# Optimization experiments

Hardware: AMD Instinct MI355X
Metric: run time of the kernel (lower is better)

The kernel has to match this reference:

```python
import jax, jax.numpy as jnp
import numpy as np

N = 100000      # nodes
E = 1600000     # edges
F_IN = 128      # num_features
H = 64          # hidden_channels
EPS = 1e-5      # batchnorm eps


def _bn(x, gamma, beta, mean, var):
    # inference-mode BatchNorm1d
    return (x - mean) * jax.lax.rsqrt(var + EPS) * gamma + beta


def setup_inputs() -> dict:
    key = jax.random.key(0)
    ks = jax.random.split(key, 16)

    def lin_w(k, fan_in, fan_out):
        return (jax.random.normal(k, (fan_in, fan_out), jnp.float32)
                * (1.0 / np.sqrt(fan_in)))

    return {
        "x": jax.random.normal(ks[0], (N, F_IN), jnp.float32),
        "edge_index": jax.random.randint(ks[1], (2, E), 0, N, dtype=jnp.int32),
        # node_encoder: Linear(F_IN,H) + BN
        "enc_W": lin_w(ks[2], F_IN, H), "enc_b": jnp.zeros((H,), jnp.float32),
        "enc_g": jnp.ones((H,), jnp.float32), "enc_beta": jnp.zeros((H,), jnp.float32),
        "enc_mean": jnp.zeros((H,), jnp.float32), "enc_var": jnp.ones((H,), jnp.float32),
        # GCNConv layers (PyG: lin without bias, bias added after aggregation)
        "conv1_W": lin_w(ks[3], H, H), "conv1_b": jnp.zeros((H,), jnp.float32),
        "conv2_W": lin_w(ks[4], H, H), "conv2_b": jnp.zeros((H,), jnp.float32),
        # edge_predictor: Linear(2H,H) + BN + Linear(H,1)
        "ep1_W": lin_w(ks[5], 2 * H, H), "ep1_b": jnp.zeros((H,), jnp.float32),
        "ep_g": jnp.ones((H,), jnp.float32), "ep_beta": jnp.zeros((H,), jnp.float32),
        "ep_mean": jnp.zeros((H,), jnp.float32), "ep_var": jnp.ones((H,), jnp.float32),
        "ep2_W": lin_w(ks[6], H, 1), "ep2_b": jnp.zeros((1,), jnp.float32),
    }


def reference(x, edge_index, enc_W, enc_b, enc_g, enc_beta, enc_mean, enc_var,
              conv1_W, conv1_b, conv2_W, conv2_b,
              ep1_W, ep1_b, ep_g, ep_beta, ep_mean, ep_var, ep2_W, ep2_b):
    row, col = edge_index[0], edge_index[1]

    # GCN normalization with added self-loops (symmetric D^-1/2 (A+I) D^-1/2)
    loops = jnp.arange(N, dtype=row.dtype)
    row_sl = jnp.concatenate([row, loops])          # [E+N]
    col_sl = jnp.concatenate([col, loops])
    deg = jax.ops.segment_sum(jnp.ones_like(col_sl, jnp.float32), col_sl, N)
    dinv = jnp.where(deg > 0, jax.lax.rsqrt(jnp.maximum(deg, 1.0)), 0.0)
    norm = dinv[row_sl] * dinv[col_sl]              # [E+N]

    def gcn_conv(h, W, b):
        hw = h @ W                                   # [N,H]
        msg = hw[row_sl] * norm[:, None]             # gather-scale  [E+N,H]
        return jax.ops.segment_sum(msg, col_sl, N) + b  # scatter-add

    # node encoder (inference: dropout = identity)
    h = jax.nn.relu(_bn(x @ enc_W + enc_b, enc_g, enc_beta, enc_mean, enc_var))
    h = jax.nn.relu(gcn_conv(h, conv1_W, conv1_b))
    h = jax.nn.relu(gcn_conv(h, conv2_W, conv2_b))
    node_embeddings = h

    # edge predictor: gather + cat + MLP + sigmoid
    ef = jnp.concatenate([h[row], h[col]], axis=1)   # [E, 2H]
    e = jax.nn.relu(_bn(ef @ ep1_W + ep1_b, ep_g, ep_beta, ep_mean, ep_var))
    edge_pred = jax.nn.sigmoid(e @ ep2_W + ep2_b)    # [E, 1]
    return node_embeddings, edge_pred
```

## Files before the change

### kernel.cpp

```cpp
#include <hip/hip_runtime.h>
#include <hip/hip_bf16.h>
#include <hip/hip_fp16.h>

#define NN 100000
#define NE 1600000
#define FIN 128
#define HD 64
#define NB_SCAN 391
#define NB_MF 1563
#define BSH 9
#define NBUCK 196
#define BCAP 10240
#define CHUNK 4096
#define NCHUNK 391
#define ESPLIT 4
#define NEB (NBUCK*ESPLIT)
#define NFB 6250

typedef unsigned int uint32;
typedef _Float16 half8 __attribute__((ext_vector_type(8)));
typedef float f32x4 __attribute__((ext_vector_type(4)));
typedef float f32x8 __attribute__((ext_vector_type(8)));

__global__ void __launch_bounds__(256) k_part(const int* __restrict__ row,
                                              const int* __restrict__ col,
                                              int* __restrict__ bcnt,
                                              uint32* __restrict__ staged,
                                              uint32* __restrict__ posE){
    __shared__ int hist[NBUCK];
    __shared__ int base[NBUCK];
    int t = threadIdx.x;
    int e0 = blockIdx.x * CHUNK;
    int e1 = min(e0 + CHUNK, NE);
    for(int i = t; i < NBUCK; i += 256) hist[i] = 0;
    __syncthreads();
    for(int e = e0 + t; e < e1; e += 256)
        atomicAdd(&hist[col[e] >> BSH], 1);
    __syncthreads();
    for(int i = t; i < NBUCK; i += 256){
        int c = hist[i];
        base[i] = (c > 0) ? atomicAdd(&bcnt[i], c) : 0;
        hist[i] = 0;
    }
    __syncthreads();
    for(int e = e0 + t; e < e1; e += 256){
        int c = col[e], r = row[e];
        int b = c >> BSH;
        int pos = base[b] + atomicAdd(&hist[b], 1);
        if(pos < BCAP){
            staged[(size_t)b*BCAP + pos] = ((uint32)r << BSH) | (uint32)(c & 511);
            posE[e] = (uint32)(b*BCAP + pos);
        } else posE[e] = 0xFFFFFFFFu;
    }
}

__global__ void __launch_bounds__(256) k_hist(const int* __restrict__ bcnt,
                                              const uint32* __restrict__ staged,
                                              int* __restrict__ deg){
    __shared__ int h[512];
    int b = blockIdx.x, t = threadIdx.x;
    for(int i = t; i < 512; i += 256) h[i] = 0;
    __syncthreads();
    int cnt = min(bcnt[b], BCAP);
    const uint32* st = staged + (size_t)b*BCAP;
    for(int i = t; i < cnt; i += 256) atomicAdd(&h[st[i] & 511u], 1);
    __syncthreads();
    for(int i = t; i < 512; i += 256){
        int n = b*512 + i;
        if(n < NN) deg[n] = h[i];
    }
}

__global__ void k_bsum(const int* __restrict__ deg, int* __restrict__ bsum){
    __shared__ int r[256];
    int t = threadIdx.x; int i = blockIdx.x*256 + t;
    r[t] = (i < NN) ? deg[i] : 0;
    __syncthreads();
    for(int off=128; off>0; off>>=1){ if(t<off) r[t]+=r[t+off]; __syncthreads(); }
    if(t==0) bsum[blockIdx.x] = r[0];
}

__global__ void k_top(int* __restrict__ bsum){
    __shared__ int s[512];
    int t = threadIdx.x;
    int v = (t < NB_SCAN) ? bsum[t] : 0;
    s[t] = v; __syncthreads();
    for(int off=1; off<512; off<<=1){
        int a = (t>=off)? s[t-off] : 0;
        __syncthreads();
        s[t] += a;
        __syncthreads();
    }
    if(t < NB_SCAN) bsum[t] = s[t] - v;
}

__global__ void k_scan(const int* __restrict__ deg, const int* __restrict__ bsum,
                       int* __restrict__ starts, float* __restrict__ dinv){
    __shared__ int s[256];
    int t = threadIdx.x; int i = blockIdx.x*256 + t;
    int d = (i<NN)? deg[i] : 0;
    s[t] = d; __syncthreads();
    for(int off=1; off<256; off<<=1){
        int a = (t>=off)? s[t-off] : 0;
        __syncthreads();
        s[t] += a;
        __syncthreads();
    }
    if(i < NN){
        starts[i] = bsum[blockIdx.x] + s[t] - d;
        dinv[i] = rsqrtf((float)(d + 1));
    }
}

__global__ void __launch_bounds__(256) k_fill2(const int* __restrict__ bcnt,
                                               const uint32* __restrict__ staged,
                                               const int* __restrict__ starts,
                                               int* __restrict__ csr){
    __shared__ int cur[512];
    __shared__ int lcsr[BCAP];
    int b = blockIdx.x, t = threadIdx.x;
    int n0 = b*512;
    int base = starts[n0];
    for(int i = t; i < 512; i += 256){
        int n = n0 + i;
        cur[i] = (n < NN) ? starts[n] - base : 0;
    }
    __syncthreads();
    int cnt = min(bcnt[b], BCAP);
    const uint32* st = staged + (size_t)b*BCAP;
    for(int i = t; i < cnt; i += 256){
        uint32 u = st[i];
        int p = atomicAdd(&cur[u & 511u], 1);
        lcsr[p] = (int)(u >> BSH);
    }
    __syncthreads();
    for(int i = t; i < cnt; i += 256) csr[base + i] = lcsr[i];
}

__global__ void k_const(const float* __restrict__ encB, const float* __restrict__ encG,
                        const float* __restrict__ encBe, const float* __restrict__ encM,
                        const float* __restrict__ encV,
                        const float* __restrict__ ep1b, const float* __restrict__ epG,
                        const float* __restrict__ epBe, const float* __restrict__ epM,
                        const float* __restrict__ epV,
                        float* __restrict__ foldEnc, float* __restrict__ foldPre){
    int j = threadIdx.x;
    if(j < 64){
        float s = encG[j]*rsqrtf(encV[j]+1e-5f);
        foldEnc[j]      = s;
        foldEnc[64+j]   = (encB[j]-encM[j])*s + encBe[j];
        float sp = epG[j]*rsqrtf(epV[j]+1e-5f);
        foldPre[j]      = sp;
        foldPre[64+j]   = sp;
        foldPre[128+j]  = sp*(ep1b[j]-epM[j]) + epBe[j];
        foldPre[192+j]  = 0.f;
    }
}

__global__ void k_wprep(const float* __restrict__ encW, const float* __restrict__ c1W,
                        const float* __restrict__ c2W, const float* __restrict__ ep1W,
                        _Float16* __restrict__ wt){
    int i = blockIdx.x*256 + threadIdx.x;
    if(i < 8192){
        int n = i >> 7, k = i & 127;
        wt[i] = (_Float16)encW[k*64 + n];
    } else if(i < 12288){
        int j = i - 8192; int n = j >> 6, k = j & 63;
        wt[i] = (_Float16)c1W[k*64 + n];
    } else if(i < 16384){
        int j = i - 12288; int n = j >> 6, k = j & 63;
        wt[i] = (_Float16)c2W[k*64 + n];
    } else if(i < 24576){
        int j = i - 16384; int h = j >> 12; int jj = j & 4095;
        int n = jj >> 6, k = jj & 63;
        wt[i] = (_Float16)ep1W[(h*64 + k)*64 + n];
    }
}

template<int K, bool AF32, bool FOLD, bool RELU, bool SCALE, int OS>
__global__ void __launch_bounds__(256) k_mfma(const void* __restrict__ Ain,
                                              const _Float16* __restrict__ Bt,
                                              const float* __restrict__ fold,
                                              const float* __restrict__ rowscale,
                                              _Float16* __restrict__ outh){
    constexpr int PS = K + 8;
    __shared__ _Float16 As[64*PS];
    __shared__ _Float16 Bs[64*PS];
    int t = threadIdx.x;
    int m0 = blockIdx.x*64;
    int jh = blockIdx.y;
    {
        const _Float16* src = Bt + (size_t)jh*64*K;
        for(int idx = t; idx < 64*(K/8); idx += 256){
            int n = idx/(K/8), c = idx%(K/8);
            *(half8*)&Bs[n*PS + c*8] = *(const half8*)&src[n*K + c*8];
        }
    }
    if(AF32){
        const float* A = (const float*)Ain;
        for(int idx = t; idx < 64*(K/4); idx += 256){
            int r = idx/(K/4), c = idx%(K/4);
            int rowi = m0 + r; if(rowi >= NN) rowi = NN-1;
            float4 v = *(const float4*)&A[(size_t)rowi*K + c*4];
            _Float16* d = &As[r*PS + c*4];
            d[0]=(_Float16)v.x; d[1]=(_Float16)v.y; d[2]=(_Float16)v.z; d[3]=(_Float16)v.w;
        }
    } else {
        const _Float16* A = (const _Float16*)Ain;
        for(int idx = t; idx < 64*(K/8); idx += 256){
            int r = idx/(K/8), c = idx%(K/8);
            int rowi = m0 + r; if(rowi >= NN) rowi = NN-1;
            *(half8*)&As[r*PS + c*8] = *(const half8*)&A[(size_t)rowi*K + c*8];
        }
    }
    __syncthreads();
    int w = t>>6, l = t&63;
    int lm = l&15, q = l>>4;
    f32x4 acc0 = {0.f,0.f,0.f,0.f}, acc1 = {0.f,0.f,0.f,0.f};
    f32x4 acc2 = {0.f,0.f,0.f,0.f}, acc3 = {0.f,0.f,0.f,0.f};
    const _Float16* arow = &As[(w*16+lm)*PS + q*8];
    const _Float16* brow = &Bs[lm*PS + q*8];
    #pragma unroll
    for(int ks = 0; ks < K/32; ks++){
        half8 a  = *(const half8*)(arow + ks*32);
        half8 b0 = *(const half8*)(brow + ks*32);
        half8 b1 = *(const half8*)(brow + 16*PS + ks*32);
        half8 b2 = *(const half8*)(brow + 32*PS + ks*32);
        half8 b3 = *(const half8*)(brow + 48*PS + ks*32);
        acc0 = __builtin_amdgcn_mfma_f32_16x16x32_f16(a, b0, acc0, 0,0,0);
        acc1 = __builtin_amdgcn_mfma_f32_16x16x32_f16(a, b1, acc1, 0,0,0);
        acc2 = __builtin_amdgcn_mfma_f32_16x16x32_f16(a, b2, acc2, 0,0,0);
        acc3 = __builtin_amdgcn_mfma_f32_16x16x32_f16(a, b3, acc3, 0,0,0);
    }
    f32x4 accs[4] = {acc0, acc1, acc2, acc3};
    #pragma unroll
    for(int nt = 0; nt < 4; nt++){
        int col = nt*16 + lm;
        int jcol = jh*64 + col;
        float fs = FOLD ? fold[jcol] : 0.f;
        float fb = FOLD ? fold[OS + jcol] : 0.f;
        #pragma unroll
        for(int r = 0; r < 4; r++){
            int rowi = m0 + w*16 + q*4 + r;
            if(rowi >= NN) continue;
            float v = accs[nt][r];
            if(FOLD) v = v*fs + fb;
            if(RELU) v = fmaxf(v, 0.f);
            if(SCALE) v *= rowscale[rowi];
            outh[(size_t)rowi*OS + jcol] = (_Float16)v;
        }
    }
}

__global__ void __launch_bounds__(256) k_agg3(const __half* __restrict__ hws,
                                              const int* __restrict__ starts,
                                              const int* __restrict__ deg,
                                              const int* __restrict__ csr,
                                              const float* __restrict__ dinv,
                                              const float* __restrict__ bias,
                                              _Float16* __restrict__ outh,
                                              float* __restrict__ outf){
    int t = threadIdx.x, w = t>>6, f = t&63;
    int n = blockIdx.x*4 + w;
    int s = __builtin_amdgcn_readfirstlane(starts[n]);
    int d = __builtin_amdgcn_readfirstlane(deg[n]);
    float acc = 0.f;
    int i = 0;
    for(; i+7 < d; i += 8){
        int r0 = csr[s+i],   r1 = csr[s+i+1];
        int r2 = csr[s+i+2], r3 = csr[s+i+3];
        int r4 = csr[s+i+4], r5 = csr[s+i+5];
        int r6 = csr[s+i+6], r7 = csr[s+i+7];
        float v0 = __half2float(hws[(size_t)r0*64 + f]);
        float v1 = __half2float(hws[(size_t)r1*64 + f]);
        float v2 = __half2float(hws[(size_t)r2*64 + f]);
        float v3 = __half2float(hws[(size_t)r3*64 + f]);
        float v4 = __half2float(hws[(size_t)r4*64 + f]);
        float v5 = __half2float(hws[(size_t)r5*64 + f]);
        float v6 = __half2float(hws[(size_t)r6*64 + f]);
        float v7 = __half2float(hws[(size_t)r7*64 + f]);
        acc += v0 + v1 + v2 + v3 + v4 + v5 + v6 + v7;
    }
    for(; i < d; i++){
        int r0 = csr[s+i];
        acc += __half2float(hws[(size_t)r0*64 + f]);
    }
    float dn = dinv[n];
    float self = __half2float(hws[(size_t)n*64 + f]);
    float v = (acc + self)*dn + bias[f];
    v = fmaxf(v, 0.f);
    outh[(size_t)n*64 + f] = (_Float16)v;
    if(outf) outf[(size_t)n*64 + f] = v;
}

__global__ void __launch_bounds__(512) k_edgeb(const int* __restrict__ bcnt,
                                               const uint32* __restrict__ staged,
                                               const _Float16* __restrict__ pre,
                                               const float* __restrict__ w2,
                                               const float* __restrict__ b2,
                                               _Float16* __restrict__ zqh){
    __shared__ half8 Bl[4096];
    int t = threadIdx.x;
    int item = ((int)blockIdx.x & 7)*98 + ((int)blockIdx.x >> 3);
    int b = item >> 2, s = item & 3;
    const _Float16* ps = pre;
    for(int idx = t; idx < 4096; idx += 512){
        int rl = idx >> 3, ch = idx & 7;
        int n = (b << 9) + rl; if(n >= NN) n = NN-1;
        Bl[rl*8 + (ch ^ (rl & 7))] = *(const half8*)(ps + (size_t)n*128 + 64 + ch*8);
    }
    __syncthreads();

    int cnt = min(bcnt[b], BCAP);
    int lo = (cnt * s) >> 2, hi = (cnt * (s+1)) >> 2;
    const uint32* st = staged + (size_t)b*BCAP;
    _Float16* zb = zqh + (size_t)b*BCAP;
    int p  = t & 7;
    int oc = t >> 3;
    f32x8 w2v = *(const f32x8*)(w2 + 8*p);
    float b2v = b2[0];

    auto edot = [&](uint32 u)->float{
        int r  = (int)(u >> BSH);
        int cl = (int)(u & 511u);
        half8 av = *(const half8*)(ps + (size_t)r*128 + 8*p);
        half8 bv = Bl[cl*8 + (p ^ (cl & 7))];
        half8 sv = av + bv;
        half8 zero8 = {};
        half8 rv = __builtin_elementwise_max(sv, zero8);
        f32x8 fv = __builtin_convertvector(rv, f32x8);
        float z;
        z  = fv[0]*w2v[0] + fv[1]*w2v[1];
        z  = fmaf(fv[2], w2v[2], z); z = fmaf(fv[3], w2v[3], z);
        z  = fmaf(fv[4], w2v[4], z); z = fmaf(fv[5], w2v[5], z);
        z  = fmaf(fv[6], w2v[6], z); z = fmaf(fv[7], w2v[7], z);
        return z;
    };

    int i = lo + oc;
    for(; i + 64 < hi; i += 128){
        uint32 u0 = st[i], u1 = st[i+64];
        float z0 = edot(u0);
        float z1 = edot(u1);
        z0 += __shfl_xor(z0, 1, 64); z1 += __shfl_xor(z1, 1, 64);
        z0 += __shfl_xor(z0, 2, 64); z1 += __shfl_xor(z1, 2, 64);
        z0 += __shfl_xor(z0, 4, 64); z1 += __shfl_xor(z1, 4, 64);
        if(p == 0){
            zb[i]    = (_Float16)(1.f/(1.f+__expf(-(z0+b2v))));
            zb[i+64] = (_Float16)(1.f/(1.f+__expf(-(z1+b2v))));
        }
    }
    for(; i < hi; i += 64){
        uint32 u0 = st[i];
        float z0 = edot(u0);
        z0 += __shfl_xor(z0, 1, 64);
        z0 += __shfl_xor(z0, 2, 64);
        z0 += __shfl_xor(z0, 4, 64);
        if(p == 0) zb[i] = (_Float16)(1.f/(1.f+__expf(-(z0+b2v))));
    }
}

__global__ void __launch_bounds__(256) k_final(const uint32* __restrict__ posE,
                                               const _Float16* __restrict__ zqh,
                                               float* __restrict__ out){
    int e = blockIdx.x*256 + threadIdx.x;
    if(e < NE){
        uint32 pz = posE[e];
        out[e] = (float)zqh[pz < (uint32)(NBUCK*BCAP) ? pz : 0u];
    }
}


extern "C" void kernel_launch(void* const* d_in, const int* in_sizes, int n_in,
                              void* d_out, int out_size, void* d_ws, size_t ws_size,
                              hipStream_t stream){
    const float* x   = (const float*)d_in[0];
    const int* ei    = (const int*)d_in[1];
    const int* row   = ei;
    const int* col   = ei + NE;
    const float* encW = (const float*)d_in[2],  *encB = (const float*)d_in[3];
    const float* encG = (const float*)d_in[4],  *encBe= (const float*)d_in[5];
    const float* encM = (const float*)d_in[6],  *encV = (const float*)d_in[7];
    const float* c1W  = (const float*)d_in[8],  *c1b  = (const float*)d_in[9];
    const float* c2W  = (const float*)d_in[10], *c2b  = (const float*)d_in[11];
    const float* ep1W = (const float*)d_in[12], *ep1b = (const float*)d_in[13];
    const float* epG  = (const float*)d_in[14], *epBe = (const float*)d_in[15];
    const float* epM  = (const float*)d_in[16], *epV  = (const float*)d_in[17];
    const float* ep2W = (const float*)d_in[18], *ep2b = (const float*)d_in[19];

    char* wsc = (char*)d_ws;
    size_t o = 0;
    auto alloc = [&](size_t bytes)->void*{
        void* p = wsc + o; o += (bytes + 255) & ~(size_t)255; return p;
    };
    int*      deg     = (int*)     alloc((size_t)NN*4);
    int*      starts  = (int*)     alloc((size_t)NN*4);
    int*      bsum    = (int*)     alloc(1024*4);
    int*      bcnt    = (int*)     alloc((size_t)NBUCK*4);
    int*      csr     = (int*)     alloc((size_t)NE*4);
    uint32*   staged  = (uint32*)  alloc((size_t)NBUCK*BCAP*4);
    float*    dinv    = (float*)   alloc((size_t)NN*4);
    float*    foldEnc = (float*)   alloc(128*4);
    float*    foldPre = (float*)   alloc(256*4);
    _Float16* wt      = (_Float16*)alloc(24576*2);
    _Float16* bufA    = (_Float16*)alloc((size_t)NN*64*2);
    _Float16* bufB    = (_Float16*)alloc((size_t)NN*64*2);
    _Float16* preh    = (_Float16*)alloc((size_t)NN*128*2);
    uint32*   posE    = (uint32*)  alloc((size_t)NE*4);
    _Float16* zqh     = (_Float16*)alloc((size_t)NBUCK*BCAP*2);

    float* outp = (float*)d_out;
    float* node_out = outp;
    float* edge_out = outp + (size_t)NN*64;

    hipMemsetAsync(bcnt, 0, (size_t)NBUCK*4, stream);
    k_part <<<NCHUNK,  256, 0, stream>>>(row, col, bcnt, staged, posE);
    k_hist <<<NBUCK,   256, 0, stream>>>(bcnt, staged, deg);
    k_bsum <<<NB_SCAN, 256, 0, stream>>>(deg, bsum);
    k_top  <<<1,       512, 0, stream>>>(bsum);
    k_scan <<<NB_SCAN, 256, 0, stream>>>(deg, bsum, starts, dinv);
    k_fill2<<<NBUCK,   256, 0, stream>>>(bcnt, staged, starts, csr);
    k_const<<<1, 64, 0, stream>>>(encB, encG, encBe, encM, encV,
                                  ep1b, epG, epBe, epM, epV, foldEnc, foldPre);
    k_wprep<<<96, 256, 0, stream>>>(encW, c1W, c2W, ep1W, wt);

    k_mfma<128,true,true,true,false,64><<<dim3(NB_MF,1), 256, 0, stream>>>
        (x, wt, foldEnc, nullptr, bufA);

    k_mfma<64,false,false,false,true,64><<<dim3(NB_MF,1), 256, 0, stream>>>
        (bufA, wt + 8192, nullptr, dinv, bufB);
    k_agg3 <<<NN/4, 256, 0, stream>>>((const __half*)bufB, starts, deg, csr, dinv, c1b,
                                      bufA, nullptr);

    k_mfma<64,false,false,false,true,64><<<dim3(NB_MF,1), 256, 0, stream>>>
        (bufA, wt + 12288, nullptr, dinv, bufB);
    k_agg3 <<<NN/4, 256, 0, stream>>>((const __half*)bufB, starts, deg, csr, dinv, c2b,
                                      bufA, node_out);

    k_mfma<64,false,true,false,false,128><<<dim3(NB_MF,2), 256, 0, stream>>>
        (bufA, wt + 16384, foldPre, nullptr, preh);

    k_edgeb<<<NEB, 512, 0, stream>>>(bcnt, staged, (const _Float16*)preh, ep2W, ep2b, zqh);
    k_final<<<NFB, 256, 0, stream>>>(posE, zqh, edge_out);
}
```

Measured before the change: 384.1 us.

## Aggregate four nodes per wavefront with lane-loaded CSR indices and readlane broadcast

The GCN aggregation kernel now gives each wavefront four destination nodes instead of one. Neighbor indices are loaded cooperatively, one per lane, and broadcast with readlane, replacing the old redundant per-lane scalar index loads. Four independent accumulators raise memory-level parallelism. Padding uses a zeroed sentinel row at index NN, so wavefronts run to the maximum degree of their four nodes, which wastes some gathers when degrees are imbalanced.

```diff
diff --git a/kernel.cpp b/kernel.cpp
--- a/kernel.cpp
+++ b/kernel.cpp
@@ -16,6 +16,7 @@
 #define ESPLIT 4
 #define NEB (NBUCK*ESPLIT)
 #define NFB 6250
+#define NAGG 6250
 
 typedef unsigned int uint32;
 typedef _Float16 half8 __attribute__((ext_vector_type(8)));
@@ -252,7 +253,7 @@
     }
 }
 
-__global__ void __launch_bounds__(256) k_agg3(const __half* __restrict__ hws,
+__global__ void __launch_bounds__(256) k_agg4(const _Float16* __restrict__ hb,
                                               const int* __restrict__ starts,
                                               const int* __restrict__ deg,
                                               const int* __restrict__ csr,
@@ -261,36 +262,59 @@
                                               _Float16* __restrict__ outh,
                                               float* __restrict__ outf){
     int t = threadIdx.x, w = t>>6, f = t&63;
-    int n = blockIdx.x*4 + w;
-    int s = __builtin_amdgcn_readfirstlane(starts[n]);
-    int d = __builtin_amdgcn_readfirstlane(deg[n]);
-    float acc = 0.f;
-    int i = 0;
-    for(; i+7 < d; i += 8){
-        int r0 = csr[s+i],   r1 = csr[s+i+1];
-        int r2 = csr[s+i+2], r3 = csr[s+i+3];
-        int r4 = csr[s+i+4], r5 = csr[s+i+5];
-        int r6 = csr[s+i+6], r7 = csr[s+i+7];
-        float v0 = __half2float(hws[(size_t)r0*64 + f]);
-        float v1 = __half2float(hws[(size_t)r1*64 + f]);
-        float v2 = __half2float(hws[(size_t)r2*64 + f]);
-        float v3 = __half2float(hws[(size_t)r3*64 + f]);
-        float v4 = __half2float(hws[(size_t)r4*64 + f]);
-        float v5 = __half2float(hws[(size_t)r5*64 + f]);
-        float v6 = __half2float(hws[(size_t)r6*64 + f]);
-        float v7 = __half2float(hws[(size_t)r7*64 + f]);
-        acc += v0 + v1 + v2 + v3 + v4 + v5 + v6 + v7;
-    }
-    for(; i < d; i++){
-        int r0 = csr[s+i];
-        acc += __half2float(hws[(size_t)r0*64 + f]);
-    }
-    float dn = dinv[n];
-    float self = __half2float(hws[(size_t)n*64 + f]);
-    float v = (acc + self)*dn + bias[f];
-    v = fmaxf(v, 0.f);
-    outh[(size_t)n*64 + f] = (_Float16)v;
-    if(outf) outf[(size_t)n*64 + f] = v;
+    int n0 = blockIdx.x*16 + w*4;
+    int s0 = __builtin_amdgcn_readfirstlane(starts[n0+0]);
+    int s1 = __builtin_amdgcn_readfirstlane(starts[n0+1]);
+    int s2 = __builtin_amdgcn_readfirstlane(starts[n0+2]);
+    int s3 = __builtin_amdgcn_readfirstlane(starts[n0+3]);
+    int d0 = __builtin_amdgcn_readfirstlane(deg[n0+0]);
+    int d1 = __builtin_amdgcn_readfirstlane(deg[n0+1]);
+    int d2 = __builtin_amdgcn_readfirstlane(deg[n0+2]);
+    int d3 = __builtin_amdgcn_readfirstlane(deg[n0+3]);
+    float a0 = 0.f, a1 = 0.f, a2 = 0.f, a3 = 0.f;
+    int dmax = max(max(d0,d1), max(d2,d3));
+    for(int i0 = 0; i0 < dmax; i0 += 64){
+        int li0 = (i0+f < d0) ? csr[s0+i0+f] : NN;
+        int li1 = (i0+f < d1) ? csr[s1+i0+f] : NN;
+        int li2 = (i0+f < d2) ? csr[s2+i0+f] : NN;
+        int li3 = (i0+f < d3) ? csr[s3+i0+f] : NN;
+        int mm = min(dmax - i0, 64);
+        for(int j = 0; j < mm; j += 8){
+            float t0 = 0.f, t1 = 0.f, t2 = 0.f, t3 = 0.f;
+            #pragma unroll
+            for(int u = 0; u < 8; u++){
+                int r0 = __builtin_amdgcn_readlane(li0, j+u);
+                int r1 = __builtin_amdgcn_readlane(li1, j+u);
+                int r2 = __builtin_amdgcn_readlane(li2, j+u);
+                int r3 = __builtin_amdgcn_readlane(li3, j+u);
+                t0 += (float)hb[(size_t)r0*64 + f];
+                t1 += (float)hb[(size_t)r1*64 + f];
+                t2 += (float)hb[(size_t)r2*64 + f];
+                t3 += (float)hb[(size_t)r3*64 + f];
+            }
+            a0 += t0; a1 += t1; a2 += t2; a3 += t3;
+        }
+    }
+    float bv = bias[f];
+    float dn0 = dinv[n0+0], dn1 = dinv[n0+1], dn2 = dinv[n0+2], dn3 = dinv[n0+3];
+    float sf0 = (float)hb[(size_t)(n0+0)*64 + f];
+    float sf1 = (float)hb[(size_t)(n0+1)*64 + f];
+    float sf2 = (float)hb[(size_t)(n0+2)*64 + f];
+    float sf3 = (float)hb[(size_t)(n0+3)*64 + f];
+    float o0 = fmaxf((a0 + sf0)*dn0 + bv, 0.f);
+    float o1 = fmaxf((a1 + sf1)*dn1 + bv, 0.f);
+    float o2 = fmaxf((a2 + sf2)*dn2 + bv, 0.f);
+    float o3 = fmaxf((a3 + sf3)*dn3 + bv, 0.f);
+    outh[(size_t)(n0+0)*64 + f] = (_Float16)o0;
+    outh[(size_t)(n0+1)*64 + f] = (_Float16)o1;
+    outh[(size_t)(n0+2)*64 + f] = (_Float16)o2;
+    outh[(size_t)(n0+3)*64 + f] = (_Float16)o3;
+    if(outf){
+        outf[(size_t)(n0+0)*64 + f] = o0;
+        outf[(size_t)(n0+1)*64 + f] = o1;
+        outf[(size_t)(n0+2)*64 + f] = o2;
+        outf[(size_t)(n0+3)*64 + f] = o3;
+    }
 }
 
 __global__ void __launch_bounds__(512) k_edgeb(const int* __restrict__ bcnt,
@@ -404,7 +428,7 @@
     float*    foldPre = (float*)   alloc(256*4);
     _Float16* wt      = (_Float16*)alloc(24576*2);
     _Float16* bufA    = (_Float16*)alloc((size_t)NN*64*2);
-    _Float16* bufB    = (_Float16*)alloc((size_t)NN*64*2);
+    _Float16* bufB    = (_Float16*)alloc((size_t)(NN+1)*64*2);
     _Float16* preh    = (_Float16*)alloc((size_t)NN*128*2);
     uint32*   posE    = (uint32*)  alloc((size_t)NE*4);
     _Float16* zqh     = (_Float16*)alloc((size_t)NBUCK*BCAP*2);
@@ -414,6 +438,7 @@
     float* edge_out = outp + (size_t)NN*64;
 
     hipMemsetAsync(bcnt, 0, (size_t)NBUCK*4, stream);
+    hipMemsetAsync(bufB + (size_t)NN*64, 0, 128, stream);
     k_part <<<NCHUNK,  256, 0, stream>>>(row, col, bcnt, staged, posE);
     k_hist <<<NBUCK,   256, 0, stream>>>(bcnt, staged, deg);
     k_bsum <<<NB_SCAN, 256, 0, stream>>>(deg, bsum);
@@ -429,12 +454,12 @@
 
     k_mfma<64,false,false,false,true,64><<<dim3(NB_MF,1), 256, 0, stream>>>
         (bufA, wt + 8192, nullptr, dinv, bufB);
-    k_agg3 <<<NN/4, 256, 0, stream>>>((const __half*)bufB, starts, deg, csr, dinv, c1b,
+    k_agg4 <<<NAGG, 256, 0, stream>>>(bufB, starts, deg, csr, dinv, c1b,
                                       bufA, nullptr);
 
     k_mfma<64,false,false,false,true,64><<<dim3(NB_MF,1), 256, 0, stream>>>
         (bufA, wt + 12288, nullptr, dinv, bufB);
-    k_agg3 <<<NN/4, 256, 0, stream>>>((const __half*)bufB, starts, deg, csr, dinv, c2b,
+    k_agg4 <<<NAGG, 256, 0, stream>>>(bufB, starts, deg, csr, dinv, c2b,
                                       bufA, node_out);
 
     k_mfma<64,false,true,false,false,128><<<dim3(NB_MF,2), 256, 0, stream>>>
```

New measurement: 355.0 us. 1.08x faster.
